# Kernel optimization log

Measured on AMD Instinct MI355X. Metric: run time of the kernel, lower is better.

## Reference

```python
import jax, jax.numpy as jnp
import numpy as np

N_NODES = 100000
N_EDGES = 3200000
F_IN = 16


def gcn_conv(x, edge_index, W, b):
    """PyG GCNConv: x' = D^{-1/2} (A + I) D^{-1/2} (x W) + b,
    with degree computed after adding self-loops."""
    n = x.shape[0]
    xw = x @ W  # [N, F_out]
    row, col = edge_index[0], edge_index[1]  # messages flow row -> col
    ones = jnp.ones(row.shape, dtype=x.dtype)
    deg = jax.ops.segment_sum(ones, col, num_segments=n) + 1.0  # +1 for self-loop
    dinv = jax.lax.rsqrt(deg)  # [N]
    norm = dinv[row] * dinv[col]  # [E]
    msg = xw[row] * norm[:, None]  # [E, F_out]
    out = jax.ops.segment_sum(msg, col, num_segments=n)
    out = out + xw * (1.0 / deg)[:, None]  # self-loop term: norm = 1/deg
    return out + b


def setup_inputs() -> dict:
    key = jax.random.key(0)
    ks = jax.random.split(key, 8)
    x = jax.random.normal(ks[0], (N_NODES, F_IN), dtype=jnp.float32)
    edge_index = jax.random.randint(ks[1], (2, N_EDGES), 0, N_NODES, dtype=jnp.int32)
    # GCNConv weights (glorot in PyG; random normal scaled for the reference)
    W1 = jax.random.normal(ks[2], (F_IN, 4), dtype=jnp.float32) * 0.3
    W2 = jax.random.normal(ks[3], (4, 2), dtype=jnp.float32) * 0.5
    W3 = jax.random.normal(ks[4], (2, 1), dtype=jnp.float32) * 0.7
    b1 = jnp.zeros((4,), jnp.float32)
    b2 = jnp.zeros((2,), jnp.float32)
    b3 = jnp.zeros((1,), jnp.float32)
    return {"x": x, "edge_index": edge_index, "W1": W1, "b1": b1,
            "W2": W2, "b2": b2, "W3": W3, "b3": b3}


def reference(x, edge_index, W1, b1, W2, b2, W3, b3):
    # encode(): GCNConv -> relu -> GCNConv -> relu -> GCNConv -> tanh
    # (dropout is identity in eval mode)
    h = jax.nn.relu(gcn_conv(x, edge_index, W1, b1))
    h = jax.nn.relu(gcn_conv(h, edge_index, W2, b2))
    return jnp.tanh(gcn_conv(h, edge_index, W3, b3))  # [N, 1]
```

## Files before the change

### kernel.cpp

```cpp
#include <hip/hip_runtime.h>
#include <math.h>


static constexpr int BLK    = 256;
static constexpr int BSHIFT = 7;
static constexpr int BCOLS  = 128;
static constexpr int NBMAX  = 1024;
static constexpr int CAP    = 5120;
static constexpr int PAD    = 16;
static constexpr int PBLK   = 512;
static constexpr int PITER  = 13;
static constexpr int PCHUNK = PBLK * PITER;
static constexpr int SBLK   = 512;
static constexpr int GBLK   = 512;

__global__ void zero_cnt_kernel(int* __restrict__ cnt, int len) {
    int i = blockIdx.x * blockDim.x + threadIdx.x;
    if (i < len) cnt[i] = 0;
}

__global__ __launch_bounds__(PBLK) void partition_kernel(
        const int* __restrict__ row, const int* __restrict__ col,
        int* __restrict__ cnt, unsigned int* __restrict__ part,
        int e, int nbuck) {
    __shared__ unsigned int   staged[PCHUNK];
    __shared__ unsigned short bkid[PCHUNK];
    __shared__ int hist[NBMAX];
    __shared__ int excl[NBMAX];
    __shared__ int gbase[NBMAX];
    __shared__ int sh[PBLK];
    const int t = (int)threadIdx.x;
    for (int j = t; j < NBMAX; j += PBLK) hist[j] = 0;
    __syncthreads();

    const int blockstart = blockIdx.x * PCHUNK;
    const int m = min(PCHUNK, e - blockstart);

    unsigned int pay[PITER];
    int bks[PITER], rnk[PITER];
#pragma unroll
    for (int i = 0; i < PITER; ++i) {
        int idx = blockstart + i * PBLK + t;
        if (idx < e) {
            int c = col[idx], r = row[idx];
            bks[i] = c >> BSHIFT;
            pay[i] = ((unsigned int)(c & (BCOLS - 1)) << 17) | (unsigned int)r;
            rnk[i] = atomicAdd(&hist[bks[i]], 1);
        } else {
            bks[i] = -1;
        }
    }
    __syncthreads();

    int a0 = hist[2 * t], a1 = hist[2 * t + 1];
    sh[t] = a0 + a1;
    __syncthreads();
    for (int off = 1; off < PBLK; off <<= 1) {
        int v = (t >= off) ? sh[t - off] : 0;
        __syncthreads();
        sh[t] += v;
        __syncthreads();
    }
    int pairExcl = sh[t] - (a0 + a1);
    excl[2 * t]     = pairExcl;
    excl[2 * t + 1] = pairExcl + a0;
    for (int j = t; j < nbuck; j += PBLK) {
        int h = hist[j];
        gbase[j] = h ? atomicAdd(&cnt[j * PAD], h) : 0;
    }
    __syncthreads();

#pragma unroll
    for (int i = 0; i < PITER; ++i) {
        if (bks[i] >= 0) {
            int pos = excl[bks[i]] + rnk[i];
            staged[pos] = pay[i];
            bkid[pos]   = (unsigned short)bks[i];
        }
    }
    __syncthreads();

    for (int k = t; k < m; k += PBLK) {
        int bk  = bkid[k];
        int off2 = gbase[bk] + (k - excl[bk]);
        if (off2 < CAP)
            part[(size_t)bk * CAP + off2] = staged[k];
    }
}

__global__ __launch_bounds__(SBLK) void sort_y1_kernel(
        unsigned int* __restrict__ part, const int* __restrict__ cnt,
        const float* __restrict__ x, const float* __restrict__ W1,
        int* __restrict__ rs, int* __restrict__ re, float* __restrict__ dinv,
        float* __restrict__ y1, int n) {
    __shared__ unsigned int   staged[CAP];
    __shared__ unsigned int   sorted[CAP];
    __shared__ unsigned short srank[CAP];
    __shared__ int hist[BCOLS];
    __shared__ int scanb[BCOLS];
    const int b = blockIdx.x;
    const int m = min(cnt[b * PAD], CAP);
    const size_t segbase = (size_t)b * CAP;

    if (threadIdx.x < BCOLS) hist[threadIdx.x] = 0;
    __syncthreads();
    for (int k = threadIdx.x; k < m; k += SBLK) {
        unsigned int v = part[segbase + k];
        staged[k] = v;
        srank[k] = (unsigned short)atomicAdd(&hist[v >> 17], 1);
    }
    __syncthreads();

    if (threadIdx.x < BCOLS) scanb[threadIdx.x] = hist[threadIdx.x];
    __syncthreads();
    for (int off = 1; off < BCOLS; off <<= 1) {
        int v = 0;
        if (threadIdx.x < BCOLS && (int)threadIdx.x >= off)
            v = scanb[threadIdx.x - off];
        __syncthreads();
        if (threadIdx.x < BCOLS) scanb[threadIdx.x] += v;
        __syncthreads();
    }

    for (int k = threadIdx.x; k < m; k += SBLK) {
        unsigned int v = staged[k];
        int lc = (int)(v >> 17);
        sorted[(scanb[lc] - hist[lc]) + (int)srank[k]] = v & 0x1FFFFu;
    }
    __syncthreads();

    for (int k = threadIdx.x; k < m; k += SBLK)
        part[segbase + k] = sorted[k];

    int lc = (int)threadIdx.x >> 2;
    int f  = (int)threadIdx.x & 3;
    int node = b * BCOLS + lc;
    if (node < n) {
        int deg = hist[lc];
        float di = rsqrtf((float)(deg + 1));
        if (f == 0) {
            int start = (int)segbase + (scanb[lc] - deg);
            rs[node] = start;
            re[node] = start + deg;
            dinv[node] = di;
        }
        const float4* x4 = (const float4*)x + (size_t)node * 4;
        float4 r0 = x4[0], r1 = x4[1], r2 = x4[2], r3 = x4[3];
        float a = 0.0f;
        a = fmaf(r0.x, W1[0 * 4 + f], a);  a = fmaf(r0.y, W1[1 * 4 + f], a);
        a = fmaf(r0.z, W1[2 * 4 + f], a);  a = fmaf(r0.w, W1[3 * 4 + f], a);
        a = fmaf(r1.x, W1[4 * 4 + f], a);  a = fmaf(r1.y, W1[5 * 4 + f], a);
        a = fmaf(r1.z, W1[6 * 4 + f], a);  a = fmaf(r1.w, W1[7 * 4 + f], a);
        a = fmaf(r2.x, W1[8 * 4 + f], a);  a = fmaf(r2.y, W1[9 * 4 + f], a);
        a = fmaf(r2.z, W1[10 * 4 + f], a); a = fmaf(r2.w, W1[11 * 4 + f], a);
        a = fmaf(r3.x, W1[12 * 4 + f], a); a = fmaf(r3.y, W1[13 * 4 + f], a);
        a = fmaf(r3.z, W1[14 * 4 + f], a); a = fmaf(r3.w, W1[15 * 4 + f], a);
        y1[node * 4 + f] = a * di;
    }
}

template <int F, int FN, int ACT, int SUBW>
__global__ __launch_bounds__(GBLK) void gather_kernel(
        const int* __restrict__ rs, const int* __restrict__ re,
        const unsigned int* __restrict__ csr,
        const float* __restrict__ y, const float* __restrict__ dinv,
        const float* __restrict__ bias, const float* __restrict__ Wn,
        float* __restrict__ outv, int n) {
    int t = blockIdx.x * GBLK + (int)threadIdx.x;
    int node = t / SUBW;
    int lane = t % SUBW;
    if (node >= n) return;
    int s = rs[node], tend = re[node];
    float acc[F];
#pragma unroll
    for (int f = 0; f < F; ++f) acc[f] = 0.0f;
    const float4* y4 = (const float4*)y;
    const float2* y2p = (const float2*)y;
    for (int k = s + lane; k < tend; k += SUBW) {
        int r = (int)csr[k];
        if constexpr (F == 4) {
            float4 a = y4[r];
            acc[0] += a.x; acc[1] += a.y; acc[2] += a.z; acc[3] += a.w;
        } else if constexpr (F == 2) {
            float2 a = y2p[r];
            acc[0] += a.x; acc[1] += a.y;
        } else {
            acc[0] += y[r];
        }
    }
#pragma unroll
    for (int off = SUBW / 2; off > 0; off >>= 1)
#pragma unroll
        for (int f = 0; f < F; ++f) acc[f] += __shfl_xor(acc[f], off);
    if (lane == 0) {
        float di = dinv[node];
        float h[F];
#pragma unroll
        for (int f = 0; f < F; ++f) {
            float z = di * (acc[f] + y[node * F + f]) + bias[f];
            if (ACT == 1) z = fmaxf(z, 0.0f);
            if (ACT == 2) z = tanhf(z);
            h[f] = z;
        }
        if constexpr (FN > 0) {
            float o[FN];
#pragma unroll
            for (int g = 0; g < FN; ++g) o[g] = 0.0f;
#pragma unroll
            for (int f = 0; f < F; ++f)
#pragma unroll
                for (int g = 0; g < FN; ++g)
                    o[g] = fmaf(h[f], Wn[f * FN + g], o[g]);
#pragma unroll
            for (int g = 0; g < FN; ++g) outv[node * FN + g] = o[g] * di;
        } else {
#pragma unroll
            for (int f = 0; f < F; ++f) outv[node * F + f] = h[f];
        }
    }
}

extern "C" void kernel_launch(void* const* d_in, const int* in_sizes, int n_in,
                              void* d_out, int out_size, void* d_ws, size_t ws_size,
                              hipStream_t stream) {
    const float* x  = (const float*)d_in[0];
    const int*   ei = (const int*)d_in[1];
    const float* W1 = (const float*)d_in[2];
    const float* b1 = (const float*)d_in[3];
    const float* W2 = (const float*)d_in[4];
    const float* b2 = (const float*)d_in[5];
    const float* W3 = (const float*)d_in[6];
    const float* b3 = (const float*)d_in[7];
    float* out = (float*)d_out;

    const int n = in_sizes[0] / 16;
    const int e = in_sizes[1] / 2;
    const int* row = ei;
    const int* col = ei + e;

    const int nbuck = (n + BCOLS - 1) / BCOLS;

    size_t off = 0;
    auto take = [&](size_t cnt_) {
        char* p = (char*)d_ws + off * 4;
        off += (cnt_ + 15) & ~(size_t)15;
        return p;
    };
    int* cnt           = (int*)take((size_t)nbuck * PAD);
    unsigned int* part = (unsigned int*)take((size_t)nbuck * CAP);
    int* rs            = (int*)take(n);
    int* re            = (int*)take(n);
    float* dinv        = (float*)take(n);
    float* y1          = (float*)take(4 * n);
    float* y2          = (float*)take(2 * n);
    float* y3          = (float*)take(n);

    zero_cnt_kernel<<<(nbuck * PAD + BLK - 1) / BLK, BLK, 0, stream>>>(cnt, nbuck * PAD);

    const int pnb = (e + PCHUNK - 1) / PCHUNK;
    partition_kernel<<<pnb, PBLK, 0, stream>>>(row, col, cnt, part, e, nbuck);

    sort_y1_kernel<<<nbuck, SBLK, 0, stream>>>(part, cnt, x, W1, rs, re, dinv, y1, n);

    constexpr int SUBW = 8;
    const int gg = (n * SUBW + GBLK - 1) / GBLK;

    gather_kernel<4, 2, 1, SUBW><<<gg, GBLK, 0, stream>>>(rs, re, part, y1, dinv, b1, W2, y2, n);
    gather_kernel<2, 1, 1, SUBW><<<gg, GBLK, 0, stream>>>(rs, re, part, y2, dinv, b2, W3, y3, n);
    gather_kernel<1, 0, 2, SUBW><<<gg, GBLK, 0, stream>>>(rs, re, part, y3, dinv, b3, nullptr, out, n);
}
```

Before: 113.3 us.

## Use wave-shuffle scan, unroll gather loop by two, memset counters

The partition kernel's block-wide Hillis-Steele scan in shared memory is replaced by a 64-lane shuffle scan plus a small cross-wave offset table, which removes most of its barriers. The gather loop is unrolled by two so each lane has two independent index and feature loads in flight. The counter-zeroing kernel is replaced by hipMemsetAsync. These are unrelated micro-optimizations that trade a little code complexity for lower latency.

Result: faster. 110.7 us (-2.3%).

```diff
diff --git a/kernel.cpp b/kernel.cpp
--- a/kernel.cpp
+++ b/kernel.cpp
@@ -2,7 +2,6 @@
 #include <math.h>
 
 
-static constexpr int BLK    = 256;
 static constexpr int BSHIFT = 7;
 static constexpr int BCOLS  = 128;
 static constexpr int NBMAX  = 1024;
@@ -14,11 +13,6 @@
 static constexpr int SBLK   = 512;
 static constexpr int GBLK   = 512;
 
-__global__ void zero_cnt_kernel(int* __restrict__ cnt, int len) {
-    int i = blockIdx.x * blockDim.x + threadIdx.x;
-    if (i < len) cnt[i] = 0;
-}
-
 __global__ __launch_bounds__(PBLK) void partition_kernel(
         const int* __restrict__ row, const int* __restrict__ col,
         int* __restrict__ cnt, unsigned int* __restrict__ part,
@@ -28,7 +22,7 @@
     __shared__ int hist[NBMAX];
     __shared__ int excl[NBMAX];
     __shared__ int gbase[NBMAX];
-    __shared__ int sh[PBLK];
+    __shared__ int wsum[8];
     const int t = (int)threadIdx.x;
     for (int j = t; j < NBMAX; j += PBLK) hist[j] = 0;
     __syncthreads();
@@ -53,17 +47,23 @@
     __syncthreads();
 
     int a0 = hist[2 * t], a1 = hist[2 * t + 1];
-    sh[t] = a0 + a1;
-    __syncthreads();
-    for (int off = 1; off < PBLK; off <<= 1) {
-        int v = (t >= off) ? sh[t - off] : 0;
-        __syncthreads();
-        sh[t] += v;
-        __syncthreads();
-    }
-    int pairExcl = sh[t] - (a0 + a1);
-    excl[2 * t]     = pairExcl;
-    excl[2 * t + 1] = pairExcl + a0;
+    int pairsum = a0 + a1;
+    int incl = pairsum;
+#pragma unroll
+    for (int d = 1; d < 64; d <<= 1) {
+        int v = __shfl_up(incl, d, 64);
+        if ((t & 63) >= d) incl += v;
+    }
+    int wid = t >> 6, lane = t & 63;
+    if (lane == 63) wsum[wid] = incl;
+    __syncthreads();
+    int woff = 0;
+#pragma unroll
+    for (int w = 0; w < 8; ++w)
+        woff += (w < wid) ? wsum[w] : 0;
+    int exclPair = woff + incl - pairsum;
+    excl[2 * t]     = exclPair;
+    excl[2 * t + 1] = exclPair + a0;
     for (int j = t; j < nbuck; j += PBLK) {
         int h = hist[j];
         gbase[j] = h ? atomicAdd(&cnt[j * PAD], h) : 0;
@@ -176,16 +176,33 @@
     for (int f = 0; f < F; ++f) acc[f] = 0.0f;
     const float4* y4 = (const float4*)y;
     const float2* y2p = (const float2*)y;
-    for (int k = s + lane; k < tend; k += SUBW) {
-        int r = (int)csr[k];
+    int k = s + lane;
+    for (; k + SUBW < tend; k += 2 * SUBW) {
+        int r0 = (int)csr[k];
+        int r1 = (int)csr[k + SUBW];
         if constexpr (F == 4) {
-            float4 a = y4[r];
-            acc[0] += a.x; acc[1] += a.y; acc[2] += a.z; acc[3] += a.w;
+            float4 a0 = y4[r0];
+            float4 a1 = y4[r1];
+            acc[0] += a0.x + a1.x; acc[1] += a0.y + a1.y;
+            acc[2] += a0.z + a1.z; acc[3] += a0.w + a1.w;
         } else if constexpr (F == 2) {
-            float2 a = y2p[r];
-            acc[0] += a.x; acc[1] += a.y;
-        } else {
-            acc[0] += y[r];
+            float2 a0 = y2p[r0];
+            float2 a1 = y2p[r1];
+            acc[0] += a0.x + a1.x; acc[1] += a0.y + a1.y;
+        } else {
+            acc[0] += y[r0] + y[r1];
+        }
+    }
+    if (k < tend) {
+        int r0 = (int)csr[k];
+        if constexpr (F == 4) {
+            float4 a0 = y4[r0];
+            acc[0] += a0.x; acc[1] += a0.y; acc[2] += a0.z; acc[3] += a0.w;
+        } else if constexpr (F == 2) {
+            float2 a0 = y2p[r0];
+            acc[0] += a0.x; acc[1] += a0.y;
+        } else {
+            acc[0] += y[r0];
         }
     }
 #pragma unroll
@@ -255,7 +272,7 @@
     float* y2          = (float*)take(2 * n);
     float* y3          = (float*)take(n);
 
-    zero_cnt_kernel<<<(nbuck * PAD + BLK - 1) / BLK, BLK, 0, stream>>>(cnt, nbuck * PAD);
+    hipMemsetAsync(cnt, 0, (size_t)nbuck * PAD * sizeof(int), stream);
 
     const int pnb = (e + PCHUNK - 1) / PCHUNK;
     partition_kernel<<<pnb, PBLK, 0, stream>>>(row, col, cnt, part, e, nbuck);
```
